# Kernel tuning notes

Hardware: AMD Instinct MI355X
Metric: run time of the kernel (lower is better)

The kernel has to match this reference:

```python
import jax, jax.numpy as jnp
import numpy as np

H = 16        # num_attention_heads
G = 16        # groups
SCALE_MIN = 0.95
SCALE_MAX = 1.05


def setup_inputs() -> dict:
    key = jax.random.key(0)
    ks = jax.random.split(key, 9)
    B, S, E = 2, 2048, 1024
    d = {
        'hidden_states': jax.random.normal(ks[0], (B, S, E), jnp.float32),
        'Wq': jax.random.normal(ks[1], (E, E), jnp.float32) * (E ** -0.5),
        'bq': jax.random.normal(ks[2], (E,), jnp.float32) * 0.02,
        'Wk': jax.random.normal(ks[3], (E, E), jnp.float32) * (E ** -0.5),
        'bk': jax.random.normal(ks[4], (E,), jnp.float32) * 0.02,
        'Wv': jax.random.normal(ks[5], (E, E), jnp.float32) * (E ** -0.5),
        'bv': jax.random.normal(ks[6], (E,), jnp.float32) * 0.02,
        'Ws': jax.random.normal(ks[7], (H * G, E), jnp.float32) * (E ** -0.5),
        'bs': jax.random.normal(ks[8], (H * G,), jnp.float32) * 0.02,
    }
    return d


def _shape_heads(x, B, S):
    # [B,S,h*D] -> [B,h,S,D]
    return x.reshape(B, S, H, -1).transpose(0, 2, 1, 3)


def reference(hidden_states, Wq, bq, Wk, bk, Wv, bv, Ws, bs):
    B, S, E = hidden_states.shape
    D = E // H            # head dim = 64
    gd = D // G           # group dim = 4

    Q = _shape_heads(hidden_states @ Wq.T + bq, B, S)   # [B,h,S,D]
    K = _shape_heads(hidden_states @ Wk.T + bk, B, S)
    V = _shape_heads(hidden_states @ Wv.T + bv, B, S)

    # groupwise dynamic scales, narrow sigmoid range
    s_logits = hidden_states @ Ws.T + bs                 # [B,S,h*g]
    s = jax.nn.sigmoid(s_logits) * (SCALE_MAX - SCALE_MIN) + SCALE_MIN
    s = s.reshape(B, S, H, G).transpose(0, 2, 1, 3)      # [B,h,S,g]
    s = jnp.repeat(s, gd, axis=-1)                       # [B,h,S,D]

    Q = Q * s  # apply_to='q'

    scores = jnp.einsum('bhsd,bhtd->bhst', Q, K) / jnp.sqrt(jnp.float32(D))
    probs = jax.nn.softmax(scores, axis=-1)
    ctx = jnp.einsum('bhst,bhtd->bhsd', probs, V)        # [B,h,S,D]
    ctx = ctx.transpose(0, 2, 1, 3).reshape(B, S, H * D)
    return ctx
```

## Files before the change

kernel.cpp:

```cpp
#include <hip/hip_runtime.h>

typedef short bf16x8 __attribute__((ext_vector_type(8)));
typedef float f32x4 __attribute__((ext_vector_type(4)));

__device__ inline float bf2f(ushort u) {
    unsigned v = ((unsigned)u) << 16;
    return __builtin_bit_cast(float, v);
}
__device__ inline ushort f2bf(float f) {
    unsigned u = __builtin_bit_cast(unsigned, f);
    u += 0x7fffu + ((u >> 16) & 1u);
    return (ushort)(u >> 16);
}
__device__ inline void async_load16(const ushort* g, ushort* l) {
    __builtin_amdgcn_global_load_lds((const __attribute__((address_space(1))) void*)g,
                                     (__attribute__((address_space(3))) void*)l, 16, 0, 0);
}

__global__ void cast_all(const float* __restrict__ hs, const float* __restrict__ Wq,
                         const float* __restrict__ Wk, const float* __restrict__ Wv,
                         const float* __restrict__ Ws,
                         ushort* __restrict__ dhs, ushort* __restrict__ dWq,
                         ushort* __restrict__ dWk, ushort* __restrict__ dWv,
                         ushort* __restrict__ dWs)
{
    int bid = blockIdx.x;
    const float* src; ushort* dst; int off;
    if (bid < 2048)      { src = hs; dst = dhs; off = bid; }
    else if (bid < 2560) { src = Wq; dst = dWq; off = bid - 2048; }
    else if (bid < 3072) { src = Wk; dst = dWk; off = bid - 2560; }
    else if (bid < 3584) { src = Wv; dst = dWv; off = bid - 3072; }
    else                 { src = Ws; dst = dWs; off = bid - 3584; }
    int i = (off * 256 + threadIdx.x) * 8;
    float4 a = *(const float4*)(src + i);
    float4 b = *(const float4*)(src + i + 4);
    union { ushort u[8]; float4 v; } o;
    o.u[0] = f2bf(a.x); o.u[1] = f2bf(a.y); o.u[2] = f2bf(a.z); o.u[3] = f2bf(a.w);
    o.u[4] = f2bf(b.x); o.u[5] = f2bf(b.y); o.u[6] = f2bf(b.z); o.u[7] = f2bf(b.w);
    *(float4*)(dst + i) = o.v;
}

__launch_bounds__(256, 4)
__global__ void fused_qkvs(const ushort* __restrict__ X,
                           const ushort* __restrict__ Wq, const ushort* __restrict__ Wk,
                           const ushort* __restrict__ Wv, const ushort* __restrict__ Ws,
                           const float* __restrict__ bq, const float* __restrict__ bk,
                           const float* __restrict__ bv, const float* __restrict__ bs,
                           ushort* __restrict__ Qb, ushort* __restrict__ Kb,
                           ushort* __restrict__ VtG, float* __restrict__ sb)
{
    __shared__ __align__(16) ushort Sm[128 * 136];
    ushort* As = Sm;
    ushort* Bs = Sm + 128 * 64;

    const int tid = threadIdx.x, w = tid >> 6, lane = tid & 63;
    const int l15 = lane & 15, quad = lane >> 4;
    const int lrow = lane >> 3;
    const int gchunk = ((lane & 7) ^ lrow) * 8;

    const int wid = blockIdx.x;
    const int r8 = wid & 7, jj = wid >> 3;
    const int by = (jj & 3) * 8 + r8;
    const int xb = jj >> 2;
    const int m0 = by * 128;

    const ushort* W; const float* bias; int n0, mode;
    if (xb < 8)       { W = Wq; bias = bq; n0 = xb * 128;        mode = 1; }
    else if (xb < 16) { W = Wk; bias = bk; n0 = (xb - 8) * 128;  mode = 0; }
    else if (xb < 24) { W = Wv; bias = bv; n0 = (xb - 16) * 128; mode = 2; }
    else              { W = Ws; bias = bs; n0 = (xb - 24) * 128; mode = 3; }

    const int wm = (w >> 1) * 64, wn = (w & 1) * 64;

    f32x4 acc[4][4];
    for (int i = 0; i < 4; i++) for (int j = 0; j < 4; j++) acc[i][j] = (f32x4){0.f, 0.f, 0.f, 0.f};

    for (int k0 = 0; k0 < 1024; k0 += 64) {
        __syncthreads();
        for (int c = 0; c < 4; ++c) {
            int r = w * 32 + c * 8;
            async_load16(&X[(size_t)(m0 + r + lrow) * 1024 + k0 + gchunk], &As[r * 64]);
            async_load16(&W[(size_t)(n0 + r + lrow) * 1024 + k0 + gchunk], &Bs[r * 64]);
        }
        __syncthreads();
        for (int kk = 0; kk < 64; kk += 32) {
            const int csw = quad + (kk >> 3);
            bf16x8 a[4], b[4];
            for (int i = 0; i < 4; i++)
                a[i] = *(const bf16x8*)&As[(wm + i * 16 + l15) * 64 + ((csw ^ (l15 & 7)) * 8)];
            for (int j = 0; j < 4; j++)
                b[j] = *(const bf16x8*)&Bs[(wn + j * 16 + l15) * 64 + ((csw ^ (l15 & 7)) * 8)];
            for (int i = 0; i < 4; i++)
                for (int j = 0; j < 4; j++)
                    acc[i][j] = __builtin_amdgcn_mfma_f32_16x16x32_bf16(a[i], b[j], acc[i][j], 0, 0, 0);
        }
    }

    const float QSCALE = 0.125f * 1.44269504f;

    if (mode == 3) {
        for (int i = 0; i < 4; i++)
            for (int j = 0; j < 4; j++) {
                int gn = n0 + wn + j * 16 + l15;
                float bv_ = bias[gn];
                for (int r = 0; r < 4; r++) {
                    int gm = m0 + wm + i * 16 + quad * 4 + r;
                    float v = acc[i][j][r] + bv_;
                    float sg = 1.0f / (1.0f + exp2f(-v * 1.44269504f));
                    sb[(size_t)gm * 256 + gn] = sg * 0.1f + 0.95f;
                }
            }
        return;
    }

    __syncthreads();

    if (mode == 2) {
        for (int i = 0; i < 4; i++)
            for (int j = 0; j < 4; j++) {
                int gnl = wn + j * 16 + l15;
                float bv_ = bias[n0 + gnl];
                ushort4 pk;
                pk.x = f2bf(acc[i][j][0] + bv_);
                pk.y = f2bf(acc[i][j][1] + bv_);
                pk.z = f2bf(acc[i][j][2] + bv_);
                pk.w = f2bf(acc[i][j][3] + bv_);
                *(ushort4*)&Sm[gnl * 136 + wm + i * 16 + quad * 4] = pk;
            }
        __syncthreads();
        const int bb = m0 >> 11, sloc = m0 & 2047;
        for (int it = 0; it < 8; ++it) {
            int d = (tid >> 4) + it * 16;
            int s8 = (tid & 15) * 8;
            float4 v = *(float4*)&Sm[d * 136 + s8];
            int h = (n0 + d) >> 6, dd = d & 63;
            *(float4*)&VtG[(size_t)(bb * 16 + h) * 131072 + (size_t)dd * 2048 + sloc + s8] = v;
        }
    } else {
        for (int i = 0; i < 4; i++)
            for (int j = 0; j < 4; j++) {
                int gnl = wn + j * 16 + l15;
                float bv_ = bias[n0 + gnl];
                for (int r = 0; r < 4; r++) {
                    float v = acc[i][j][r] + bv_;
                    if (mode == 1) v *= QSCALE;
                    Sm[(wm + i * 16 + quad * 4 + r) * 136 + gnl] = f2bf(v);
                }
            }
        __syncthreads();
        ushort* dst = (mode == 1) ? Qb : Kb;
        for (int it = 0; it < 8; ++it) {
            int row = (tid >> 4) + it * 16, c = (tid & 15) * 8;
            *(float4*)&dst[(size_t)(m0 + row) * 1024 + n0 + c] = *(float4*)&Sm[row * 136 + c];
        }
    }
}

__launch_bounds__(256, 3)
__global__ void attn_kernel(const ushort* __restrict__ Q, const ushort* __restrict__ K,
                            const ushort* __restrict__ Vt, const float* __restrict__ sb,
                            float* __restrict__ out)
{
    __shared__ __align__(16) ushort SmA[4 * 64 * 64];
    __shared__ __align__(16) ushort Ps[4 * 32 * 64];
    ushort* Ks0 = SmA;
    ushort* Ks1 = SmA + 4096;
    ushort* Vs0 = SmA + 8192;
    ushort* Vs1 = SmA + 12288;
    ushort* Qs  = SmA;

    const int tid = threadIdx.x, w = tid >> 6, lane = tid & 63;
    const int l15 = lane & 15, quad = lane >> 4;
    const int lrow = lane >> 3;
    const int gchunk = ((lane & 7) ^ lrow) * 8;

    const int wid = blockIdx.x;
    const int r8 = wid & 7, jj = wid >> 3;
    const int bh = (jj & 3) * 8 + r8;
    const int qx = jj >> 2;
    const int b = bh >> 4, h = bh & 15;
    const int q0 = qx * 128;
    const size_t rowbase = (size_t)b * 2048;
    const int cbase = h * 64;

    for (int it = 0; it < 4; ++it) {
        int l = tid + it * 256;
        int r = l >> 3, c = (l & 7) * 8;
        union { float4 f; ushort u[8]; } uu, oo;
        uu.f = *(const float4*)&Q[(rowbase + q0 + r) * 1024 + cbase + c];
        const float* sp = &sb[(rowbase + q0 + r) * 256 + ((cbase + c) >> 2)];
        float s0 = sp[0], s1 = sp[1];
        for (int j = 0; j < 4; j++) oo.u[j] = f2bf(bf2f(uu.u[j]) * s0);
        for (int j = 4; j < 8; j++) oo.u[j] = f2bf(bf2f(uu.u[j]) * s1);
        *(float4*)&Qs[r * 72 + c] = oo.f;
    }
    __syncthreads();

    bf16x8 aq[2][2];
    for (int mt = 0; mt < 2; mt++)
        for (int kk2 = 0; kk2 < 2; kk2++)
            aq[mt][kk2] = *(const bf16x8*)&Qs[(w * 32 + mt * 16 + l15) * 72 + kk2 * 32 + quad * 8];
    __syncthreads();

    for (int c = 0; c < 2; ++c) {
        int r = w * 16 + c * 8;
        async_load16(&K[(rowbase + r + lrow) * 1024 + cbase + gchunk], &Ks0[r * 64]);
        async_load16(&Vt[(size_t)bh * 131072 + (size_t)(r + lrow) * 2048 + gchunk], &Vs0[r * 64]);
    }

    ushort* pw = &Ps[w * 2048 + l15 * 64 + ((quad >> 1) ^ (l15 & 7) & 1 ? 0 : 0)]; (void)pw;
    const int wrbase = w * 2048 + l15 * 64 + (quad & 1) * 4;
    const int rdbase = w * 2048 + l15 * 64;

    float lsum[2] = {0.f, 0.f};
    f32x4 o[2][4];
    for (int mt = 0; mt < 2; mt++) for (int nt = 0; nt < 4; nt++) o[mt][nt] = (f32x4){0.f, 0.f, 0.f, 0.f};
    const f32x4 z4 = (f32x4){0.f, 0.f, 0.f, 0.f};

#define ATTN_STEP(KC, VC, KN, VN, KT, PREFETCH)                                                         \
    {                                                                                                   \
        __syncthreads();                       \
        if (PREFETCH) {                                                                                 \
            int nk = (KT) + 1;                                                                          \
            for (int c = 0; c < 2; ++c) {                                                               \
                int r = w * 16 + c * 8;                                                                 \
                async_load16(&K[(rowbase + nk * 64 + r + lrow) * 1024 + cbase + gchunk], &KN[r * 64]);  \
                async_load16(&Vt[(size_t)bh * 131072 + (size_t)(r + lrow) * 2048 + nk * 64 + gchunk],   \
                             &VN[r * 64]);                                                              \
            }                                                                                           \
        }                                                                                               \
        bf16x8 kb[2][4], vb[2][4];                                                                      \
        for (int kk2 = 0; kk2 < 2; kk2++)                                                               \
            for (int nt = 0; nt < 4; nt++) {                                                            \
                const int csw = ((quad + kk2 * 4) ^ (l15 & 7)) * 8;                                     \
                kb[kk2][nt] = *(const bf16x8*)&KC[(nt * 16 + l15) * 64 + csw];                          \
                vb[kk2][nt] = *(const bf16x8*)&VC[(nt * 16 + l15) * 64 + csw];                          \
            }                                                                                           \
                              \
        f32x4 st[2][4];                                                                                 \
        for (int mt = 0; mt < 2; mt++)                                                                  \
            for (int kt2 = 0; kt2 < 4; kt2++) {                                                         \
                st[mt][kt2] = __builtin_amdgcn_mfma_f32_16x16x32_bf16(kb[0][kt2], aq[mt][0], z4, 0, 0, 0); \
                st[mt][kt2] = __builtin_amdgcn_mfma_f32_16x16x32_bf16(kb[1][kt2], aq[mt][1],            \
                                                                      st[mt][kt2], 0, 0, 0);            \
            }                                                                                           \
        for (int mt = 0; mt < 2; mt++)                                                                  \
            for (int kt2 = 0; kt2 < 4; kt2++) {                                                         \
                float p0 = exp2f(st[mt][kt2][0]);                                                       \
                float p1 = exp2f(st[mt][kt2][1]);                                                       \
                float p2 = exp2f(st[mt][kt2][2]);                                                       \
                float p3 = exp2f(st[mt][kt2][3]);                                                       \
                lsum[mt] += (p0 + p1) + (p2 + p3);                                                      \
                unsigned d0 = __builtin_amdgcn_perm(__builtin_bit_cast(unsigned, p1) + 0x8000u,         \
                                                    __builtin_bit_cast(unsigned, p0) + 0x8000u,         \
                                                    0x07060302u);                                       \
                unsigned d1 = __builtin_amdgcn_perm(__builtin_bit_cast(unsigned, p3) + 0x8000u,         \
                                                    __builtin_bit_cast(unsigned, p2) + 0x8000u,         \
                                                    0x07060302u);                                       \
                uint2 pk; pk.x = d0; pk.y = d1;                                                         \
                *(uint2*)&Ps[wrbase + mt * 1024 + (((kt2 * 2 + (quad >> 1)) ^ (l15 & 7)) * 8)] = pk;    \
            }                                                                                           \
                                     \
        for (int half = 0; half < 2; half++) {                                                          \
            bf16x8 a_[2];                                                                               \
            for (int mt = 0; mt < 2; mt++)                                                              \
                a_[mt] = *(const bf16x8*)&Ps[rdbase + mt * 1024 + (((half * 4 + quad) ^ (l15 & 7)) * 8)];\
            for (int mt = 0; mt < 2; mt++)                                                              \
                for (int nt = 0; nt < 4; nt++)                                                          \
                    o[mt][nt] = __builtin_amdgcn_mfma_f32_16x16x32_bf16(a_[mt], vb[half][nt],           \
                                                                        o[mt][nt], 0, 0, 0);            \
        }                                                                                               \
    }

    for (int kt = 0; kt < 32; kt += 2) {
        ATTN_STEP(Ks0, Vs0, Ks1, Vs1, kt, 1);
        ATTN_STEP(Ks1, Vs1, Ks0, Vs0, kt + 1, (kt + 2 < 32));
    }
#undef ATTN_STEP

    float inv[2];
    for (int mt = 0; mt < 2; mt++) {
        float s = lsum[mt];
        s += __shfl_xor(s, 16);
        s += __shfl_xor(s, 32);
        inv[mt] = 1.0f / s;
    }

    for (int mt = 0; mt < 2; mt++) {
        for (int r = 0; r < 4; r++) {
            float iv = __shfl(inv[mt], quad * 4 + r);
            int q = q0 + w * 32 + mt * 16 + quad * 4 + r;
            size_t base = (rowbase + q) * 1024 + cbase;
            for (int nt = 0; nt < 4; nt++)
                out[base + nt * 16 + l15] = o[mt][nt][r] * iv;
        }
    }
}

extern "C" void kernel_launch(void* const* d_in, const int* in_sizes, int n_in,
                              void* d_out, int out_size, void* d_ws, size_t ws_size,
                              hipStream_t stream) {
    const float* hs = (const float*)d_in[0];
    const float* Wq = (const float*)d_in[1];
    const float* bq = (const float*)d_in[2];
    const float* Wk = (const float*)d_in[3];
    const float* bk = (const float*)d_in[4];
    const float* Wv = (const float*)d_in[5];
    const float* bv = (const float*)d_in[6];
    const float* Ws = (const float*)d_in[7];
    const float* bs = (const float*)d_in[8];
    float* outp = (float*)d_out;

    char* ws = (char*)d_ws;
    ushort* Qb    = (ushort*)(ws);
    ushort* Kb    = (ushort*)(ws + 8388608);
    ushort* VtG   = (ushort*)(ws + 16777216);
    float*  sb    = (float* )(ws + 25165824);
    ushort* hs_bf = (ushort*)(ws + 29360128);
    ushort* Wq_bf = (ushort*)(ws + 37748736);
    ushort* Wk_bf = (ushort*)(ws + 39845888);
    ushort* Wv_bf = (ushort*)(ws + 41943040);
    ushort* Ws_bf = (ushort*)(ws + 44040192);

    dim3 blk(256);
    cast_all<<<dim3(3712), blk, 0, stream>>>(hs, Wq, Wk, Wv, Ws,
                                             hs_bf, Wq_bf, Wk_bf, Wv_bf, Ws_bf);
    fused_qkvs<<<dim3(832), blk, 0, stream>>>(hs_bf, Wq_bf, Wk_bf, Wv_bf, Ws_bf,
                                              bq, bk, bv, bs, Qb, Kb, VtG, sb);
    attn_kernel<<<dim3(512), blk, 0, stream>>>(Qb, Kb, VtG, sb, outp);
}
```

Baseline: 186.3 us.

## Halve attention block to 128 threads with 64-query tiles and swizzled Q staging

The attention kernel moves from 256-thread blocks over 128 queries to 128-thread blocks over 64 queries, doubling the grid to 1024 blocks. Q is staged in the P buffer with an XOR swizzle, so the first K/V tile load can be issued before Q staging instead of after. LDS address offsets are precomputed outside the loop, and exp2f/reciprocal calls are replaced with the hardware intrinsics. Smaller blocks improve tail balance and occupancy, but each K/V tile is reused by fewer queries, which adds global/L2 traffic.

```diff
diff --git a/kernel.cpp b/kernel.cpp
--- a/kernel.cpp
+++ b/kernel.cpp
@@ -106,7 +106,7 @@
                 for (int r = 0; r < 4; r++) {
                     int gm = m0 + wm + i * 16 + quad * 4 + r;
                     float v = acc[i][j][r] + bv_;
-                    float sg = 1.0f / (1.0f + exp2f(-v * 1.44269504f));
+                    float sg = __builtin_amdgcn_rcpf(1.0f + __builtin_amdgcn_exp2f(-v * 1.44269504f));
                     sb[(size_t)gm * 256 + gn] = sg * 0.1f + 0.95f;
                 }
             }
@@ -156,18 +156,18 @@
     }
 }
 
-__launch_bounds__(256, 3)
+__launch_bounds__(128, 2)
 __global__ void attn_kernel(const ushort* __restrict__ Q, const ushort* __restrict__ K,
                             const ushort* __restrict__ Vt, const float* __restrict__ sb,
                             float* __restrict__ out)
 {
-    __shared__ __align__(16) ushort SmA[4 * 64 * 64];
-    __shared__ __align__(16) ushort Ps[4 * 32 * 64];
+    __shared__ __align__(16) ushort SmA[4 * 4096];
+    __shared__ __align__(16) ushort Ps[4096];
     ushort* Ks0 = SmA;
     ushort* Ks1 = SmA + 4096;
     ushort* Vs0 = SmA + 8192;
     ushort* Vs1 = SmA + 12288;
-    ushort* Qs  = SmA;
+    ushort* Qs  = Ps;
 
     const int tid = threadIdx.x, w = tid >> 6, lane = tid & 63;
     const int l15 = lane & 15, quad = lane >> 4;
@@ -179,38 +179,54 @@
     const int bh = (jj & 3) * 8 + r8;
     const int qx = jj >> 2;
     const int b = bh >> 4, h = bh & 15;
-    const int q0 = qx * 128;
+    const int q0 = qx * 64;
     const size_t rowbase = (size_t)b * 2048;
     const int cbase = h * 64;
 
+    const ushort* kg = K + (rowbase + w * 32 + lrow) * 1024 + cbase + gchunk;
+    const ushort* vg = Vt + (size_t)bh * 131072 + (size_t)(w * 32 + lrow) * 2048 + gchunk;
+
+    for (int c = 0; c < 4; ++c) {
+        async_load16(kg + c * 8192,  Ks0 + w * 2048 + c * 512);
+        async_load16(vg + c * 16384, Vs0 + w * 2048 + c * 512);
+    }
+
     for (int it = 0; it < 4; ++it) {
-        int l = tid + it * 256;
-        int r = l >> 3, c = (l & 7) * 8;
+        int l = tid + it * 128;
+        int r = l >> 3, ch = l & 7;
+        int c = ch * 8;
         union { float4 f; ushort u[8]; } uu, oo;
         uu.f = *(const float4*)&Q[(rowbase + q0 + r) * 1024 + cbase + c];
         const float* sp = &sb[(rowbase + q0 + r) * 256 + ((cbase + c) >> 2)];
         float s0 = sp[0], s1 = sp[1];
         for (int j = 0; j < 4; j++) oo.u[j] = f2bf(bf2f(uu.u[j]) * s0);
         for (int j = 4; j < 8; j++) oo.u[j] = f2bf(bf2f(uu.u[j]) * s1);
-        *(float4*)&Qs[r * 72 + c] = oo.f;
+        *(float4*)&Qs[r * 64 + ((ch ^ (r & 7)) * 8)] = oo.f;
     }
     __syncthreads();
 
     bf16x8 aq[2][2];
     for (int mt = 0; mt < 2; mt++)
         for (int kk2 = 0; kk2 < 2; kk2++)
-            aq[mt][kk2] = *(const bf16x8*)&Qs[(w * 32 + mt * 16 + l15) * 72 + kk2 * 32 + quad * 8];
+            aq[mt][kk2] = *(const bf16x8*)&Qs[(w * 32 + mt * 16 + l15) * 64
+                                              + (((kk2 * 4 + quad) ^ (l15 & 7)) * 8)];
     __syncthreads();
 
-    for (int c = 0; c < 2; ++c) {
-        int r = w * 16 + c * 8;
-        async_load16(&K[(rowbase + r + lrow) * 1024 + cbase + gchunk], &Ks0[r * 64]);
-        async_load16(&Vt[(size_t)bh * 131072 + (size_t)(r + lrow) * 2048 + gchunk], &Vs0[r * 64]);
-    }
-
-    ushort* pw = &Ps[w * 2048 + l15 * 64 + ((quad >> 1) ^ (l15 & 7) & 1 ? 0 : 0)]; (void)pw;
-    const int wrbase = w * 2048 + l15 * 64 + (quad & 1) * 4;
-    const int rdbase = w * 2048 + l15 * 64;
+    int kvoff[2][4];
+    for (int kk2 = 0; kk2 < 2; kk2++)
+        for (int nt = 0; nt < 4; nt++)
+            kvoff[kk2][nt] = (nt * 16 + l15) * 64 + (((quad + kk2 * 4) ^ (l15 & 7)) * 8);
+    int wroff[2][4], rdoff[2][2];
+    {
+        const int wrb = w * 2048 + l15 * 64 + (quad & 1) * 4;
+        const int rdb = w * 2048 + l15 * 64;
+        for (int mt = 0; mt < 2; mt++) {
+            for (int kt2 = 0; kt2 < 4; kt2++)
+                wroff[mt][kt2] = wrb + mt * 1024 + (((kt2 * 2 + (quad >> 1)) ^ (l15 & 7)) * 8);
+            for (int half = 0; half < 2; half++)
+                rdoff[mt][half] = rdb + mt * 1024 + (((half * 4 + quad) ^ (l15 & 7)) * 8);
+        }
+    }
 
     float lsum[2] = {0.f, 0.f};
     f32x4 o[2][4];
@@ -221,22 +237,19 @@
     {                                                                                                   \
         __syncthreads();                       \
         if (PREFETCH) {                                                                                 \
-            int nk = (KT) + 1;                                                                          \
-            for (int c = 0; c < 2; ++c) {                                                               \
-                int r = w * 16 + c * 8;                                                                 \
-                async_load16(&K[(rowbase + nk * 64 + r + lrow) * 1024 + cbase + gchunk], &KN[r * 64]);  \
-                async_load16(&Vt[(size_t)bh * 131072 + (size_t)(r + lrow) * 2048 + nk * 64 + gchunk],   \
-                             &VN[r * 64]);                                                              \
+            const int nk = (KT) + 1;                                                                    \
+            for (int c = 0; c < 4; ++c) {                                                               \
+                async_load16(kg + nk * 65536 + c * 8192, KN + w * 2048 + c * 512);                      \
+                async_load16(vg + nk * 64 + c * 16384,   VN + w * 2048 + c * 512);                      \
             }                                                                                           \
         }                                                                                               \
         bf16x8 kb[2][4], vb[2][4];                                                                      \
         for (int kk2 = 0; kk2 < 2; kk2++)                                                               \
             for (int nt = 0; nt < 4; nt++) {                                                            \
-                const int csw = ((quad + kk2 * 4) ^ (l15 & 7)) * 8;                                     \
-                kb[kk2][nt] = *(const bf16x8*)&KC[(nt * 16 + l15) * 64 + csw];                          \
-                vb[kk2][nt] = *(const bf16x8*)&VC[(nt * 16 + l15) * 64 + csw];                          \
+                kb[kk2][nt] = *(const bf16x8*)&KC[kvoff[kk2][nt]];                                      \
+                vb[kk2][nt] = *(const bf16x8*)&VC[kvoff[kk2][nt]];                                      \
             }                                                                                           \
-                              \
+                                                     \
         f32x4 st[2][4];                                                                                 \
         for (int mt = 0; mt < 2; mt++)                                                                  \
             for (int kt2 = 0; kt2 < 4; kt2++) {                                                         \
@@ -246,10 +259,10 @@
             }                                                                                           \
         for (int mt = 0; mt < 2; mt++)                                                                  \
             for (int kt2 = 0; kt2 < 4; kt2++) {                                                         \
-                float p0 = exp2f(st[mt][kt2][0]);                                                       \
-                float p1 = exp2f(st[mt][kt2][1]);                                                       \
-                float p2 = exp2f(st[mt][kt2][2]);                                                       \
-                float p3 = exp2f(st[mt][kt2][3]);                                                       \
+                float p0 = __builtin_amdgcn_exp2f(st[mt][kt2][0]);                                      \
+                float p1 = __builtin_amdgcn_exp2f(st[mt][kt2][1]);                                      \
+                float p2 = __builtin_amdgcn_exp2f(st[mt][kt2][2]);                                      \
+                float p3 = __builtin_amdgcn_exp2f(st[mt][kt2][3]);                                      \
                 lsum[mt] += (p0 + p1) + (p2 + p3);                                                      \
                 unsigned d0 = __builtin_amdgcn_perm(__builtin_bit_cast(unsigned, p1) + 0x8000u,         \
                                                     __builtin_bit_cast(unsigned, p0) + 0x8000u,         \
@@ -258,13 +271,13 @@
                                                     __builtin_bit_cast(unsigned, p2) + 0x8000u,         \
                                                     0x07060302u);                                       \
                 uint2 pk; pk.x = d0; pk.y = d1;                                                         \
-                *(uint2*)&Ps[wrbase + mt * 1024 + (((kt2 * 2 + (quad >> 1)) ^ (l15 & 7)) * 8)] = pk;    \
+                *(uint2*)&Ps[wroff[mt][kt2]] = pk;                                                      \
             }                                                                                           \
                                      \
         for (int half = 0; half < 2; half++) {                                                          \
             bf16x8 a_[2];                                                                               \
             for (int mt = 0; mt < 2; mt++)                                                              \
-                a_[mt] = *(const bf16x8*)&Ps[rdbase + mt * 1024 + (((half * 4 + quad) ^ (l15 & 7)) * 8)];\
+                a_[mt] = *(const bf16x8*)&Ps[rdoff[mt][half]];                                          \
             for (int mt = 0; mt < 2; mt++)                                                              \
                 for (int nt = 0; nt < 4; nt++)                                                          \
                     o[mt][nt] = __builtin_amdgcn_mfma_f32_16x16x32_bf16(a_[mt], vb[half][nt],           \
@@ -322,10 +335,9 @@
     ushort* Wv_bf = (ushort*)(ws + 41943040);
     ushort* Ws_bf = (ushort*)(ws + 44040192);
 
-    dim3 blk(256);
-    cast_all<<<dim3(3712), blk, 0, stream>>>(hs, Wq, Wk, Wv, Ws,
-                                             hs_bf, Wq_bf, Wk_bf, Wv_bf, Ws_bf);
-    fused_qkvs<<<dim3(832), blk, 0, stream>>>(hs_bf, Wq_bf, Wk_bf, Wv_bf, Ws_bf,
-                                              bq, bk, bv, bs, Qb, Kb, VtG, sb);
-    attn_kernel<<<dim3(512), blk, 0, stream>>>(Qb, Kb, VtG, sb, outp);
-}
+    cast_all<<<dim3(3712), dim3(256), 0, stream>>>(hs, Wq, Wk, Wv, Ws,
+                                                   hs_bf, Wq_bf, Wk_bf, Wv_bf, Ws_bf);
+    fused_qkvs<<<dim3(832), dim3(256), 0, stream>>>(hs_bf, Wq_bf, Wk_bf, Wv_bf, Ws_bf,
+                                                    bq, bk, bv, bs, Qb, Kb, VtG, sb);
+    attn_kernel<<<dim3(1024), dim3(128), 0, stream>>>(Qb, Kb, VtG, sb, outp);
+}
```

Result: faster. 180.3 us (-3.2%).
